# Optimization experiments

Hardware: AMD Instinct MI355X
Metric: run time of the kernel (lower is better)

## Reference

```python
import jax, jax.numpy as jnp
import numpy as np


def _apply_rope(q, k):
    # q, k: [BH, T, hd]
    hd = q.shape[-1]
    half = hd // 2
    T = q.shape[1]
    inv_freq = 1.0 / (10000.0 ** (jnp.arange(half, dtype=jnp.float32) / half))
    freqs = jnp.arange(T, dtype=jnp.float32)[:, None] * inv_freq[None, :]  # [T, half]
    cos = jnp.cos(freqs)[None, :, :]
    sin = jnp.sin(freqs)[None, :, :]
    q1, q2 = q[..., :half], q[..., half:]
    k1, k2 = k[..., :half], k[..., half:]
    q_rot = jnp.concatenate([q1 * cos - q2 * sin, q1 * sin + q2 * cos], axis=-1)
    k_rot = jnp.concatenate([k1 * cos - k2 * sin, k1 * sin + k2 * cos], axis=-1)
    return q_rot, k_rot


def setup_inputs() -> dict:
    key = jax.random.key(0)
    ks = jax.random.split(key, 5)
    B, T, D = 2, 2048, 1024
    x = jax.random.normal(ks[0], (B, T, D), dtype=jnp.float32)
    w_qkv = jax.random.normal(ks[1], (D, 3 * D), dtype=jnp.float32) * (1.0 / np.sqrt(D))
    b_qkv = jax.random.normal(ks[2], (3 * D,), dtype=jnp.float32) * 0.01
    w_out = jax.random.normal(ks[3], (D, D), dtype=jnp.float32) * (1.0 / np.sqrt(D))
    b_out = jax.random.normal(ks[4], (D,), dtype=jnp.float32) * 0.01
    return {"x": x, "w_qkv": w_qkv, "b_qkv": b_qkv, "w_out": w_out, "b_out": b_out}


def reference(x, w_qkv, b_qkv, w_out, b_out):
    B, T, D = x.shape
    H = 16
    hd = D // H
    qkv = x @ w_qkv + b_qkv  # [B, T, 3D]
    q, k, v = jnp.split(qkv, 3, axis=-1)
    # [B, T, H, hd] -> [B, H, T, hd]
    q = q.reshape(B, T, H, hd).transpose(0, 2, 1, 3)
    k = k.reshape(B, T, H, hd).transpose(0, 2, 1, 3)
    v = v.reshape(B, T, H, hd).transpose(0, 2, 1, 3)
    q, k = _apply_rope(q.reshape(B * H, T, hd), k.reshape(B * H, T, hd))
    q = q.reshape(B, H, T, hd)
    k = k.reshape(B, H, T, hd)
    scores = jnp.einsum("bhqd,bhkd->bhqk", q, k) / jnp.sqrt(jnp.float32(hd))
    attn = jax.nn.softmax(scores, axis=-1)
    out = jnp.einsum("bhqk,bhkd->bhqd", attn, v)  # [B, H, T, hd]
    out = out.transpose(0, 2, 1, 3).reshape(B, T, D)
    return out @ w_out + b_out
```

## Files before the change

### kernel.cpp

```cpp
#include <hip/hip_runtime.h>
#include <hip/hip_bf16.h>
#include <stdint.h>


typedef __bf16 bf16;
typedef __bf16 bf16x8 __attribute__((ext_vector_type(8)));
typedef __bf16 bf16x4 __attribute__((ext_vector_type(4)));
typedef float  f32x4  __attribute__((ext_vector_type(4)));

__device__ __forceinline__ void gload16(void* lds, const void* g) {
  __builtin_amdgcn_global_load_lds((__attribute__((address_space(1))) void*)(void*)g,
                                   (__attribute__((address_space(3))) void*)lds, 16, 0, 0);
}


__global__ void k_convert_x(const float* __restrict__ x, bf16* __restrict__ xb, int n) {
  int i = (blockIdx.x * blockDim.x + threadIdx.x) * 4;
  if (i >= n) return;
  float4 v = *(const float4*)(x + i);
  bf16x4 o;
  o.x = (bf16)v.x; o.y = (bf16)v.y; o.z = (bf16)v.z; o.w = (bf16)v.w;
  *(bf16x4*)(xb + i) = o;
}

__global__ void k_transpose_bf16(const float* __restrict__ in, bf16* __restrict__ out,
                                 int rows, int cols) {
  __shared__ float t[32][33];
  int c0 = blockIdx.x * 32, r0 = blockIdx.y * 32;
  for (int i = threadIdx.y; i < 32; i += 8)
    t[i][threadIdx.x] = in[(size_t)(r0 + i) * cols + c0 + threadIdx.x];
  __syncthreads();
  for (int i = threadIdx.y; i < 32; i += 8)
    out[(size_t)(c0 + i) * rows + r0 + threadIdx.x] = (bf16)t[threadIdx.x][i];
}


__global__ __launch_bounds__(256)
void k_gemm_qkv(const bf16* __restrict__ A, const bf16* __restrict__ Bt,
                const float* __restrict__ bias, bf16* __restrict__ Qd,
                bf16* __restrict__ Kd, bf16* __restrict__ Vtd) {
  alignas(16) __shared__ bf16 lds_a[128 * 32];
  alignas(16) __shared__ bf16 lds_b[128 * 32];
  const int tid = threadIdx.x;
  const int lane = tid & 63, w = tid >> 6;
  const int wr = w >> 1, wc = w & 1;
  const int bid = blockIdx.x;
  const int swz = (bid & 7) * 96 + (bid >> 3);
  const int br = swz / 24, bc = swz % 24;
  const int r16 = lane & 15, g4 = lane >> 4;

  f32x4 acc[4][4] = {};
  const bf16* gA = A + (size_t)(br * 128 + (lane >> 2)) * 1024 + (lane & 3) * 8;
  const bf16* gB = Bt + (size_t)(bc * 128 + (lane >> 2)) * 1024 + (lane & 3) * 8;

  for (int kt = 0; kt < 32; ++kt) {
    const int ko = kt * 32;
#pragma unroll
    for (int it = 0; it < 2; ++it) {
      const int row0 = 16 * (4 * it + w);
      gload16(&lds_a[row0 * 32], gA + (size_t)row0 * 1024 + ko);
      gload16(&lds_b[row0 * 32], gB + (size_t)row0 * 1024 + ko);
    }
    __syncthreads();
    bf16x8 af[4], bfr[4];
#pragma unroll
    for (int m = 0; m < 4; ++m)
      af[m] = *(const bf16x8*)&lds_a[(wr * 64 + 16 * m + r16) * 32 + g4 * 8];
#pragma unroll
    for (int n = 0; n < 4; ++n)
      bfr[n] = *(const bf16x8*)&lds_b[(wc * 64 + 16 * n + r16) * 32 + g4 * 8];
#pragma unroll
    for (int m = 0; m < 4; ++m)
#pragma unroll
      for (int n = 0; n < 4; ++n)
        acc[m][n] = __builtin_amdgcn_mfma_f32_16x16x32_bf16(af[m], bfr[n], acc[m][n], 0, 0, 0);
    __syncthreads();
  }

  const int reg = bc >> 3;
  const int h = ((bc & 7) << 1) | wc;
  const float bq = 0.125f * 1.4426950408889634f;
  const float Lc = 13.287712379549449f / 32.0f;
  const float if0 = exp2f(-(float)r16 * Lc);
  const float if1 = exp2f(-(float)(16 + r16) * Lc);
  float bv[4];
#pragma unroll
  for (int n = 0; n < 4; ++n) bv[n] = bias[bc * 128 + wc * 64 + 16 * n + r16];

  if (reg == 2) {
#pragma unroll
    for (int m = 0; m < 4; ++m) {
      const int row0 = br * 128 + wr * 64 + 16 * m + 4 * g4;
      const int t0 = row0 & 2047, b = row0 >> 11;
      const int pos = (t0 & ~63) | (((t0 >> 2) & 3) << 4) | (((t0 >> 5) & 1) << 3) |
                      (((t0 >> 4) & 1) << 2);
#pragma unroll
      for (int n = 0; n < 4; ++n) {
        bf16x4 pk;
#pragma unroll
        for (int r = 0; r < 4; ++r) pk[r] = (bf16)(acc[m][n][r] + bv[n]);
        *(bf16x4*)(Vtd + ((size_t)((b * 16 + h) * 64) + 16 * n + r16) * 2048 + pos) = pk;
      }
    }
  } else {
    bf16* dst = (reg == 0) ? Qd : Kd;
#pragma unroll
    for (int m = 0; m < 4; ++m) {
#pragma unroll
      for (int r = 0; r < 4; ++r) {
        const int row = br * 128 + wr * 64 + 16 * m + 4 * g4 + r;
        const int t = row & 2047, b = row >> 11;
        bf16* o = dst + ((size_t)(b * 16 + h) * 2048 + t) * 64;
        const float v0 = acc[m][0][r] + bv[0];
        const float v1 = acc[m][1][r] + bv[1];
        const float v2 = acc[m][2][r] + bv[2];
        const float v3 = acc[m][3][r] + bv[3];
        float s0, c0, s1, c1;
        const float tf = (float)t;
        sincosf(tf * if0, &s0, &c0);
        sincosf(tf * if1, &s1, &c1);
        float r0 = v0 * c0 - v2 * s0, r2 = v0 * s0 + v2 * c0;
        float r1 = v1 * c1 - v3 * s1, r3 = v1 * s1 + v3 * c1;
        if (reg == 0) { r0 *= bq; r1 *= bq; r2 *= bq; r3 *= bq; }
        o[r16]      = (bf16)r0;
        o[16 + r16] = (bf16)r1;
        o[32 + r16] = (bf16)r2;
        o[48 + r16] = (bf16)r3;
      }
    }
  }
}


__global__ __launch_bounds__(256)
void k_gemm_out(const bf16* __restrict__ A, const bf16* __restrict__ Bt,
                const float* __restrict__ bias, float* __restrict__ Cp,
                int M, int N, int K) {
  alignas(16) __shared__ bf16 lds_a[128 * 32];
  alignas(16) __shared__ bf16 lds_b[128 * 32];
  const int tid = threadIdx.x;
  const int lane = tid & 63, w = tid >> 6;
  const int wr = w >> 1, wc = w & 1;
  const int nb = N >> 7;
  const int nwg = gridDim.x;
  const int bid = blockIdx.x;
  const int swz = (bid & 7) * (nwg >> 3) + (bid >> 3);
  const int br = swz / nb, bc = swz % nb;
  const int r16 = lane & 15, g4 = lane >> 4;

  f32x4 acc[4][4] = {};
  const int nk = K >> 5;
  const bf16* gA = A + (size_t)(br * 128 + (lane >> 2)) * K + (lane & 3) * 8;
  const bf16* gB = Bt + (size_t)(bc * 128 + (lane >> 2)) * K + (lane & 3) * 8;

  for (int kt = 0; kt < nk; ++kt) {
    const int ko = kt * 32;
#pragma unroll
    for (int it = 0; it < 2; ++it) {
      const int row0 = 16 * (4 * it + w);
      gload16(&lds_a[row0 * 32], gA + (size_t)row0 * K + ko);
      gload16(&lds_b[row0 * 32], gB + (size_t)row0 * K + ko);
    }
    __syncthreads();
    bf16x8 af[4], bfr[4];
#pragma unroll
    for (int m = 0; m < 4; ++m)
      af[m] = *(const bf16x8*)&lds_a[(wr * 64 + 16 * m + r16) * 32 + g4 * 8];
#pragma unroll
    for (int n = 0; n < 4; ++n)
      bfr[n] = *(const bf16x8*)&lds_b[(wc * 64 + 16 * n + r16) * 32 + g4 * 8];
#pragma unroll
    for (int m = 0; m < 4; ++m)
#pragma unroll
      for (int n = 0; n < 4; ++n)
        acc[m][n] = __builtin_amdgcn_mfma_f32_16x16x32_bf16(af[m], bfr[n], acc[m][n], 0, 0, 0);
    __syncthreads();
  }

#pragma unroll
  for (int m = 0; m < 4; ++m) {
    const int row = br * 128 + wr * 64 + 16 * m + 4 * g4;
#pragma unroll
    for (int n = 0; n < 4; ++n) {
      const int col = bc * 128 + wc * 64 + 16 * n + r16;
      const float bvv = bias[col];
#pragma unroll
      for (int r = 0; r < 4; ++r)
        Cp[(size_t)(row + r) * N + col] = acc[m][n][r] + bvv;
    }
  }
}


__global__ __launch_bounds__(256)
void k_attn(const bf16* __restrict__ Qg, const bf16* __restrict__ Kg,
            const bf16* __restrict__ Vtg, bf16* __restrict__ PO,
            float* __restrict__ lsum) {
  alignas(16) __shared__ bf16 kbuf[2][4096];
  alignas(16) __shared__ bf16 vbuf[2][4096];
  const int tid = threadIdx.x, lane = tid & 63, w = tid >> 6;
  const int bid = blockIdx.x;
  const int swz = (bid & 7) * 128 + (bid >> 3);
  const int half = swz & 1;
  const int id2 = swz >> 1;
  const int bh = id2 >> 4, q0 = (id2 & 15) * 128;
  const int r16 = lane & 15, g4 = lane >> 4;
  const char* Kb  = (const char*)(Kg  + (size_t)bh * 2048 * 64);
  const char* Vtb = (const char*)(Vtg + (size_t)bh * 64 * 2048);
  const bf16* Qb  = Qg + (size_t)bh * 2048 * 64;

  const int rl = lane >> 3;
  const int colx = ((lane & 7) * 16) ^ (rl << 4);

  bf16x8 qf[2][2];
#pragma unroll
  for (int g = 0; g < 2; ++g) {
    const int qrow = q0 + 64 * g + 16 * w + r16;
    qf[g][0] = *(const bf16x8*)(Qb + (size_t)qrow * 64 + g4 * 8);
    qf[g][1] = *(const bf16x8*)(Qb + (size_t)qrow * 64 + 32 + g4 * 8);
  }

  f32x4 O[2][4] = {};
  f32x4 O4[2] = {};
  bf16x8 ones8 = {};
  if (r16 == 0)
#pragma unroll
    for (int j = 0; j < 8; ++j) ones8[j] = (bf16)1.f;

#define STAGE(bufi, t0)                                                          \
  {                                                                              \
    _Pragma("unroll")                                                            \
    for (int c = 0; c < 2; ++c) {                                                \
      const int row = 16 * w + 8 * c + rl;                                       \
      gload16(&kbuf[bufi][(2 * w + c) * 512],                                    \
              Kb + (size_t)((t0) + row) * 128 + colx);                           \
      gload16(&vbuf[bufi][(2 * w + c) * 512],                                    \
              Vtb + (size_t)row * 4096 + (size_t)(t0) * 2 + colx);               \
    }                                                                            \
  }

  const int it0 = half * 16;
  STAGE(0, it0 * 64);
  __syncthreads();

  const int rsw = (r16 & 7) << 4;

#pragma unroll 1
  for (int ii = 0; ii < 16; ++ii) {
    const int bsel = ii & 1;
    if (ii + 1 < 16) STAGE(bsel ^ 1, (it0 + ii + 1) * 64);
    const char* kb = (const char*)kbuf[bsel] + r16 * 128;
    const char* vb = (const char*)vbuf[bsel] + r16 * 128;

    f32x4 S0[4], S1[4];
#pragma unroll
    for (int n = 0; n < 4; ++n) {
      bf16x8 kb0 = *(const bf16x8*)(kb + n * 2048 + ((g4 * 16) ^ rsw));
      bf16x8 kb1 = *(const bf16x8*)(kb + n * 2048 + ((64 + g4 * 16) ^ rsw));
      f32x4 s = {};
      s = __builtin_amdgcn_mfma_f32_16x16x32_bf16(kb0, qf[0][0], s, 0, 0, 0);
      s = __builtin_amdgcn_mfma_f32_16x16x32_bf16(kb1, qf[0][1], s, 0, 0, 0);
      S0[n] = s;
      f32x4 t = {};
      t = __builtin_amdgcn_mfma_f32_16x16x32_bf16(kb0, qf[1][0], t, 0, 0, 0);
      t = __builtin_amdgcn_mfma_f32_16x16x32_bf16(kb1, qf[1][1], t, 0, 0, 0);
      S1[n] = t;
    }

    bf16x8 pb0[2], pb1[2];
#pragma unroll
    for (int n = 0; n < 4; ++n)
#pragma unroll
      for (int r = 0; r < 4; ++r) {
        pb0[n >> 1][(n & 1) * 4 + r] = (bf16)exp2f(S0[n][r]);
        pb1[n >> 1][(n & 1) * 4 + r] = (bf16)exp2f(S1[n][r]);
      }

#pragma unroll
    for (int dn = 0; dn < 4; ++dn) {
      bf16x8 v0 = *(const bf16x8*)(vb + dn * 2048 + ((32 * g4) ^ rsw));
      bf16x8 v1 = *(const bf16x8*)(vb + dn * 2048 + ((32 * g4 + 16) ^ rsw));
      O[0][dn] = __builtin_amdgcn_mfma_f32_16x16x32_bf16(v0, pb0[0], O[0][dn], 0, 0, 0);
      O[0][dn] = __builtin_amdgcn_mfma_f32_16x16x32_bf16(v1, pb0[1], O[0][dn], 0, 0, 0);
      O[1][dn] = __builtin_amdgcn_mfma_f32_16x16x32_bf16(v0, pb1[0], O[1][dn], 0, 0, 0);
      O[1][dn] = __builtin_amdgcn_mfma_f32_16x16x32_bf16(v1, pb1[1], O[1][dn], 0, 0, 0);
    }
    O4[0] = __builtin_amdgcn_mfma_f32_16x16x32_bf16(ones8, pb0[0], O4[0], 0, 0, 0);
    O4[0] = __builtin_amdgcn_mfma_f32_16x16x32_bf16(ones8, pb0[1], O4[0], 0, 0, 0);
    O4[1] = __builtin_amdgcn_mfma_f32_16x16x32_bf16(ones8, pb1[0], O4[1], 0, 0, 0);
    O4[1] = __builtin_amdgcn_mfma_f32_16x16x32_bf16(ones8, pb1[1], O4[1], 0, 0, 0);
    __syncthreads();
  }
#undef STAGE

  bf16* POh = PO + (size_t)half * 4194304;
#pragma unroll
  for (int g = 0; g < 2; ++g) {
    const int row = bh * 2048 + q0 + 64 * g + 16 * w + r16;
#pragma unroll
    for (int n = 0; n < 4; ++n) {
      bf16x4 ov;
#pragma unroll
      for (int r = 0; r < 4; ++r) ov[r] = (bf16)O[g][n][r];
      *(bf16x4*)(POh + (size_t)row * 64 + 16 * n + 4 * g4) = ov;
    }
    if (g4 == 0) lsum[half * 65536 + row] = O4[g][0];
  }
}


__global__ __launch_bounds__(256)
void k_combine(const bf16* __restrict__ PO, const float* __restrict__ lsum,
               bf16* __restrict__ attnb) {
  const int idx = blockIdx.x * 256 + threadIdx.x;
  const int row = idx >> 3, seg = idx & 7;
  const float inv = 1.f / (lsum[row] + lsum[65536 + row]);
  bf16x8 p0 = *(const bf16x8*)(PO + (size_t)row * 64 + seg * 8);
  bf16x8 p1 = *(const bf16x8*)(PO + 4194304 + (size_t)row * 64 + seg * 8);
  bf16x8 o;
#pragma unroll
  for (int j = 0; j < 8; ++j)
    o[j] = (bf16)(((float)p0[j] + (float)p1[j]) * inv);
  const int bh = row >> 11, t = row & 2047;
  const int b = bh >> 4, h = bh & 15;
  *(bf16x8*)(attnb + ((size_t)(b * 2048 + t)) * 1024 + h * 64 + seg * 8) = o;
}


extern "C" void kernel_launch(void* const* d_in, const int* in_sizes, int n_in,
                              void* d_out, int out_size, void* d_ws, size_t ws_size,
                              hipStream_t stream) {
  const float* x     = (const float*)d_in[0];
  const float* w_qkv = (const float*)d_in[1];
  const float* b_qkv = (const float*)d_in[2];
  const float* w_out = (const float*)d_in[3];
  const float* b_out = (const float*)d_in[4];
  float* out = (float*)d_out;

  char* ws = (char*)d_ws;
  bf16* xb    = (bf16*)(ws);
  bf16* wqkvT = (bf16*)(ws + 8388608);
  bf16* Qb    = (bf16*)(ws + 16777216);
  bf16* Kb    = (bf16*)(ws + 25165824);
  bf16* Vtb   = (bf16*)(ws + 33554432);
  bf16* attnb = (bf16*)(ws + 41943040);
  bf16* woutT = (bf16*)(ws + 50331648);
  float* lsum = (float*)(ws + 52428800);
  bf16* PO    = (bf16*)(ws);

  k_convert_x<<<4096 * 1024 / 4 / 256, 256, 0, stream>>>(x, xb, 4096 * 1024);
  k_transpose_bf16<<<dim3(3072 / 32, 1024 / 32), dim3(32, 8), 0, stream>>>(w_qkv, wqkvT, 1024, 3072);
  k_transpose_bf16<<<dim3(1024 / 32, 1024 / 32), dim3(32, 8), 0, stream>>>(w_out, woutT, 1024, 1024);
  k_gemm_qkv<<<32 * 24, 256, 0, stream>>>(xb, wqkvT, b_qkv, Qb, Kb, Vtb);
  k_attn<<<1024, 256, 0, stream>>>(Qb, Kb, Vtb, PO, lsum);
  k_combine<<<2048, 256, 0, stream>>>(PO, lsum, attnb);
  k_gemm_out<<<32 * 8, 256, 0, stream>>>(attnb, woutT, b_out, out, 4096, 1024, 1024);
}
```

Measured before the change: 140.5 us.

## Split attention key tiles across wave pairs and use hardware sin/cos for RoPE

The attention kernel now handles 64 query rows per block instead of 128 and launches twice as many blocks. Each pair of waves shares the same query rows and splits every 64-key tile in half. The partial outputs and row sums are combined through shared memory before being written. This is meant to raise parallelism and occupancy, and each wave now issues half as many score and PV MFMAs per tile. In exchange, every K/V tile is loaded from global memory twice as often, and there is an extra LDS reduction at the end. Separately, RoPE swaps sincosf for range-reduced __builtin_amdgcn_sinf/cosf, which is cheaper but slightly less precise.

```diff
diff --git a/kernel.cpp b/kernel.cpp
--- a/kernel.cpp
+++ b/kernel.cpp
@@ -81,8 +81,9 @@
   const int h = ((bc & 7) << 1) | wc;
   const float bq = 0.125f * 1.4426950408889634f;
   const float Lc = 13.287712379549449f / 32.0f;
-  const float if0 = exp2f(-(float)r16 * Lc);
-  const float if1 = exp2f(-(float)(16 + r16) * Lc);
+  const float inv2pi = 0.15915494309189535f;
+  const float if0r = exp2f(-(float)r16 * Lc) * inv2pi;
+  const float if1r = exp2f(-(float)(16 + r16) * Lc) * inv2pi;
   float bv[4];
 #pragma unroll
   for (int n = 0; n < 4; ++n) bv[n] = bias[bc * 128 + wc * 64 + 16 * n + r16];
@@ -115,10 +116,11 @@
         const float v1 = acc[m][1][r] + bv[1];
         const float v2 = acc[m][2][r] + bv[2];
         const float v3 = acc[m][3][r] + bv[3];
-        float s0, c0, s1, c1;
         const float tf = (float)t;
-        sincosf(tf * if0, &s0, &c0);
-        sincosf(tf * if1, &s1, &c1);
+        float rv0 = tf * if0r; rv0 -= floorf(rv0);
+        float rv1 = tf * if1r; rv1 -= floorf(rv1);
+        const float s0 = __builtin_amdgcn_sinf(rv0), c0 = __builtin_amdgcn_cosf(rv0);
+        const float s1 = __builtin_amdgcn_sinf(rv1), c1 = __builtin_amdgcn_cosf(rv1);
         float r0 = v0 * c0 - v2 * s0, r2 = v0 * s0 + v2 * c0;
         float r1 = v1 * c1 - v3 * s1, r3 = v1 * s1 + v3 * c1;
         if (reg == 0) { r0 *= bq; r1 *= bq; r2 *= bq; r3 *= bq; }
@@ -196,14 +198,16 @@
 void k_attn(const bf16* __restrict__ Qg, const bf16* __restrict__ Kg,
             const bf16* __restrict__ Vtg, bf16* __restrict__ PO,
             float* __restrict__ lsum) {
-  alignas(16) __shared__ bf16 kbuf[2][4096];
-  alignas(16) __shared__ bf16 vbuf[2][4096];
+  alignas(16) __shared__ char smem[32768];
+  bf16* kbufs = (bf16*)smem;
+  bf16* vbufs = (bf16*)(smem + 16384);
   const int tid = threadIdx.x, lane = tid & 63, w = tid >> 6;
   const int bid = blockIdx.x;
-  const int swz = (bid & 7) * 128 + (bid >> 3);
+  const int swz = (bid & 7) * 256 + (bid >> 3);
   const int half = swz & 1;
   const int id2 = swz >> 1;
-  const int bh = id2 >> 4, q0 = (id2 & 15) * 128;
+  const int bh = id2 >> 5, q0 = (id2 & 31) * 64;
+  const int qh = w >> 1, kh = w & 1;
   const int r16 = lane & 15, g4 = lane >> 4;
   const char* Kb  = (const char*)(Kg  + (size_t)bh * 2048 * 64);
   const char* Vtb = (const char*)(Vtg + (size_t)bh * 64 * 2048);
@@ -215,7 +219,7 @@
   bf16x8 qf[2][2];
 #pragma unroll
   for (int g = 0; g < 2; ++g) {
-    const int qrow = q0 + 64 * g + 16 * w + r16;
+    const int qrow = q0 + 32 * qh + 16 * g + r16;
     qf[g][0] = *(const bf16x8*)(Qb + (size_t)qrow * 64 + g4 * 8);
     qf[g][1] = *(const bf16x8*)(Qb + (size_t)qrow * 64 + 32 + g4 * 8);
   }
@@ -232,9 +236,9 @@
     _Pragma("unroll")                                                            \
     for (int c = 0; c < 2; ++c) {                                                \
       const int row = 16 * w + 8 * c + rl;                                       \
-      gload16(&kbuf[bufi][(2 * w + c) * 512],                                    \
+      gload16(&kbufs[(bufi) * 4096 + (2 * w + c) * 512],                         \
               Kb + (size_t)((t0) + row) * 128 + colx);                           \
-      gload16(&vbuf[bufi][(2 * w + c) * 512],                                    \
+      gload16(&vbufs[(bufi) * 4096 + (2 * w + c) * 512],                         \
               Vtb + (size_t)row * 4096 + (size_t)(t0) * 2 + colx);               \
     }                                                                            \
   }
@@ -249,62 +253,75 @@
   for (int ii = 0; ii < 16; ++ii) {
     const int bsel = ii & 1;
     if (ii + 1 < 16) STAGE(bsel ^ 1, (it0 + ii + 1) * 64);
-    const char* kb = (const char*)kbuf[bsel] + r16 * 128;
-    const char* vb = (const char*)vbuf[bsel] + r16 * 128;
-
-    f32x4 S0[4], S1[4];
-#pragma unroll
-    for (int n = 0; n < 4; ++n) {
-      bf16x8 kb0 = *(const bf16x8*)(kb + n * 2048 + ((g4 * 16) ^ rsw));
-      bf16x8 kb1 = *(const bf16x8*)(kb + n * 2048 + ((64 + g4 * 16) ^ rsw));
+    const char* kb = (const char*)kbufs + bsel * 8192 + r16 * 128;
+    const char* vb = (const char*)vbufs + bsel * 8192 + r16 * 128;
+
+    f32x4 S[2][2];
+#pragma unroll
+    for (int nl = 0; nl < 2; ++nl) {
+      const int n = 2 * kh + nl;
+      bf16x8 kf0 = *(const bf16x8*)(kb + n * 2048 + ((g4 * 16) ^ rsw));
+      bf16x8 kf1 = *(const bf16x8*)(kb + n * 2048 + ((64 + g4 * 16) ^ rsw));
       f32x4 s = {};
-      s = __builtin_amdgcn_mfma_f32_16x16x32_bf16(kb0, qf[0][0], s, 0, 0, 0);
-      s = __builtin_amdgcn_mfma_f32_16x16x32_bf16(kb1, qf[0][1], s, 0, 0, 0);
-      S0[n] = s;
+      s = __builtin_amdgcn_mfma_f32_16x16x32_bf16(kf0, qf[0][0], s, 0, 0, 0);
+      s = __builtin_amdgcn_mfma_f32_16x16x32_bf16(kf1, qf[0][1], s, 0, 0, 0);
+      S[0][nl] = s;
       f32x4 t = {};
-      t = __builtin_amdgcn_mfma_f32_16x16x32_bf16(kb0, qf[1][0], t, 0, 0, 0);
-      t = __builtin_amdgcn_mfma_f32_16x16x32_bf16(kb1, qf[1][1], t, 0, 0, 0);
-      S1[n] = t;
-    }
-
-    bf16x8 pb0[2], pb1[2];
-#pragma unroll
-    for (int n = 0; n < 4; ++n)
-#pragma unroll
-      for (int r = 0; r < 4; ++r) {
-        pb0[n >> 1][(n & 1) * 4 + r] = (bf16)exp2f(S0[n][r]);
-        pb1[n >> 1][(n & 1) * 4 + r] = (bf16)exp2f(S1[n][r]);
+      t = __builtin_amdgcn_mfma_f32_16x16x32_bf16(kf0, qf[1][0], t, 0, 0, 0);
+      t = __builtin_amdgcn_mfma_f32_16x16x32_bf16(kf1, qf[1][1], t, 0, 0, 0);
+      S[1][nl] = t;
+    }
+
+    bf16x8 pb[2];
+#pragma unroll
+    for (int g = 0; g < 2; ++g)
+#pragma unroll
+      for (int nl = 0; nl < 2; ++nl)
+#pragma unroll
+        for (int r = 0; r < 4; ++r)
+          pb[g][nl * 4 + r] = (bf16)exp2f(S[g][nl][r]);
+
+#pragma unroll
+    for (int dn = 0; dn < 4; ++dn) {
+      bf16x8 vf = *(const bf16x8*)(vb + dn * 2048 + ((32 * g4 + 16 * kh) ^ rsw));
+      O[0][dn] = __builtin_amdgcn_mfma_f32_16x16x32_bf16(vf, pb[0], O[0][dn], 0, 0, 0);
+      O[1][dn] = __builtin_amdgcn_mfma_f32_16x16x32_bf16(vf, pb[1], O[1][dn], 0, 0, 0);
+    }
+    O4[0] = __builtin_amdgcn_mfma_f32_16x16x32_bf16(ones8, pb[0], O4[0], 0, 0, 0);
+    O4[1] = __builtin_amdgcn_mfma_f32_16x16x32_bf16(ones8, pb[1], O4[1], 0, 0, 0);
+    __syncthreads();
+  }
+#undef STAGE
+
+  float* obuf = (float*)smem;
+  float* lbuf = (float*)(smem + 17408);
+  if (kh == 1) {
+#pragma unroll
+    for (int g = 0; g < 2; ++g) {
+#pragma unroll
+      for (int dn = 0; dn < 4; ++dn)
+        *(f32x4*)&obuf[(qh * 32 + g * 16 + r16) * 68 + 16 * dn + 4 * g4] = O[g][dn];
+      if (g4 == 0) lbuf[qh * 32 + g * 16 + r16] = O4[g][0];
+    }
+  }
+  __syncthreads();
+  if (kh == 0) {
+    bf16* POh = PO + (size_t)half * 4194304;
+#pragma unroll
+    for (int g = 0; g < 2; ++g) {
+      const int row = bh * 2048 + q0 + 32 * qh + 16 * g + r16;
+      const float ls = __shfl(O4[g][0], r16, 64) + lbuf[qh * 32 + g * 16 + r16];
+#pragma unroll
+      for (int dn = 0; dn < 4; ++dn) {
+        f32x4 os = O[g][dn];
+        f32x4 ot = *(const f32x4*)&obuf[(qh * 32 + g * 16 + r16) * 68 + 16 * dn + 4 * g4];
+        bf16x4 ov;
+#pragma unroll
+        for (int r = 0; r < 4; ++r) ov[r] = (bf16)(os[r] + ot[r]);
+        *(bf16x4*)(POh + (size_t)row * 64 + 16 * dn + 4 * g4) = ov;
       }
-
-#pragma unroll
-    for (int dn = 0; dn < 4; ++dn) {
-      bf16x8 v0 = *(const bf16x8*)(vb + dn * 2048 + ((32 * g4) ^ rsw));
-      bf16x8 v1 = *(const bf16x8*)(vb + dn * 2048 + ((32 * g4 + 16) ^ rsw));
-      O[0][dn] = __builtin_amdgcn_mfma_f32_16x16x32_bf16(v0, pb0[0], O[0][dn], 0, 0, 0);
-      O[0][dn] = __builtin_amdgcn_mfma_f32_16x16x32_bf16(v1, pb0[1], O[0][dn], 0, 0, 0);
-      O[1][dn] = __builtin_amdgcn_mfma_f32_16x16x32_bf16(v0, pb1[0], O[1][dn], 0, 0, 0);
-      O[1][dn] = __builtin_amdgcn_mfma_f32_16x16x32_bf16(v1, pb1[1], O[1][dn], 0, 0, 0);
-    }
-    O4[0] = __builtin_amdgcn_mfma_f32_16x16x32_bf16(ones8, pb0[0], O4[0], 0, 0, 0);
-    O4[0] = __builtin_amdgcn_mfma_f32_16x16x32_bf16(ones8, pb0[1], O4[0], 0, 0, 0);
-    O4[1] = __builtin_amdgcn_mfma_f32_16x16x32_bf16(ones8, pb1[0], O4[1], 0, 0, 0);
-    O4[1] = __builtin_amdgcn_mfma_f32_16x16x32_bf16(ones8, pb1[1], O4[1], 0, 0, 0);
-    __syncthreads();
-  }
-#undef STAGE
-
-  bf16* POh = PO + (size_t)half * 4194304;
-#pragma unroll
-  for (int g = 0; g < 2; ++g) {
-    const int row = bh * 2048 + q0 + 64 * g + 16 * w + r16;
-#pragma unroll
-    for (int n = 0; n < 4; ++n) {
-      bf16x4 ov;
-#pragma unroll
-      for (int r = 0; r < 4; ++r) ov[r] = (bf16)O[g][n][r];
-      *(bf16x4*)(POh + (size_t)row * 64 + 16 * n + 4 * g4) = ov;
-    }
-    if (g4 == 0) lsum[half * 65536 + row] = O4[g][0];
+      if (g4 == 0) lsum[half * 65536 + row] = ls;
+    }
   }
 }
 
@@ -352,7 +369,7 @@
   k_transpose_bf16<<<dim3(3072 / 32, 1024 / 32), dim3(32, 8), 0, stream>>>(w_qkv, wqkvT, 1024, 3072);
   k_transpose_bf16<<<dim3(1024 / 32, 1024 / 32), dim3(32, 8), 0, stream>>>(w_out, woutT, 1024, 1024);
   k_gemm_qkv<<<32 * 24, 256, 0, stream>>>(xb, wqkvT, b_qkv, Qb, Kb, Vtb);
-  k_attn<<<1024, 256, 0, stream>>>(Qb, Kb, Vtb, PO, lsum);
+  k_attn<<<2048, 256, 0, stream>>>(Qb, Kb, Vtb, PO, lsum);
   k_combine<<<2048, 256, 0, stream>>>(PO, lsum, attnb);
   k_gemm_out<<<32 * 8, 256, 0, stream>>>(attnb, woutT, b_out, out, 4096, 1024, 1024);
 }
```

Result: faster. 137.5 us (-2.1%).
